# Kernel tuning notes

Measured on AMD Instinct MI355X. Metric: run time of the kernel, lower is better.

## Reference

```python
import jax, jax.numpy as jnp
import numpy as np

# Phi-3-small blocksparse config
S = 2048            # num prompt tokens (single sequence)
H = 32              # num query heads
HKV = 8             # num kv heads (GQA)
D = 128             # head size
BLK = 64            # sparse_block_size
LOCAL = 16          # local_blocks
VERT = 8            # vert_stride
SCALE = 0.08838834764831845  # 1/sqrt(128)
HEAD_SLIDE = max(1, VERT // H)  # = 1 (per-head vertical offset, homo_head=False)


def _blocksparse_mask():
    """Per-head local+strided block-sparse causal mask, shape [H, S, S] bool."""
    nb = S // BLK
    qb = jnp.arange(nb)[None, :, None]   # query block idx
    kb = jnp.arange(nb)[None, None, :]   # key block idx
    h = jnp.arange(H)[:, None, None]
    blk = (qb >= kb) & (
        (qb - kb < LOCAL) | (((kb + h * HEAD_SLIDE + 1) % VERT) == 0)
    )  # [H, nb, nb]
    dense = jnp.repeat(jnp.repeat(blk, BLK, axis=1), BLK, axis=2)  # [H, S, S]
    causal = jnp.arange(S)[:, None] >= jnp.arange(S)[None, :]
    return dense & causal[None]


def setup_inputs() -> dict:
    key = jax.random.key(0)
    k1, k2, k3 = jax.random.split(key, 3)
    return {
        "query": jax.random.normal(k1, (S, H * D), dtype=jnp.float32),
        "key": jax.random.normal(k2, (S, HKV * D), dtype=jnp.float32),
        "value": jax.random.normal(k3, (S, HKV * D), dtype=jnp.float32),
    }


def reference(query, key, value):
    q = query.reshape(S, H, D)
    k = jnp.repeat(key.reshape(S, HKV, D), H // HKV, axis=1)    # GQA expand
    v = jnp.repeat(value.reshape(S, HKV, D), H // HKV, axis=1)
    scores = jnp.einsum("qhd,khd->hqk", q, k) * SCALE           # [H, S, S]
    mask = _blocksparse_mask()
    scores = jnp.where(mask, scores, jnp.finfo(scores.dtype).min)
    p = jax.nn.softmax(scores, axis=-1)
    out = jnp.einsum("hqk,khd->qhd", p, v)                      # [S, H, D]
    return out.reshape(S, H * D)
```

## Files before the change

kernel.cpp:

```cpp
#include <hip/hip_runtime.h>


typedef __bf16 bf16_t;
typedef __bf16 bf16x4 __attribute__((ext_vector_type(4)));
typedef __bf16 bf16x8 __attribute__((ext_vector_type(8)));
typedef float  fx4    __attribute__((ext_vector_type(4)));

#define SL2E_F 0.1275240614354876f

__device__ inline void load_lds16(const bf16_t* g, bf16_t* l) {
    __builtin_amdgcn_global_load_lds(
        (const __attribute__((address_space(1))) void*)g,
        (__attribute__((address_space(3))) void*)l, 16, 0, 0);
}

__global__ void prep_kernel(const float* __restrict__ K, const float* __restrict__ V,
                            bf16_t* __restrict__ Kb, bf16_t* __restrict__ VT)
{
    const int blk = blockIdx.x;
    {
        const size_t base = (size_t)blk * 4096 + (size_t)threadIdx.x * 16;
        fx4 a0 = *(const fx4*)(K + base);
        fx4 a1 = *(const fx4*)(K + base + 4);
        fx4 a2 = *(const fx4*)(K + base + 8);
        fx4 a3 = *(const fx4*)(K + base + 12);
        bf16x8 f0, f1;
        f0[0]=(bf16_t)a0[0]; f0[1]=(bf16_t)a0[1]; f0[2]=(bf16_t)a0[2]; f0[3]=(bf16_t)a0[3];
        f0[4]=(bf16_t)a1[0]; f0[5]=(bf16_t)a1[1]; f0[6]=(bf16_t)a1[2]; f0[7]=(bf16_t)a1[3];
        f1[0]=(bf16_t)a2[0]; f1[1]=(bf16_t)a2[1]; f1[2]=(bf16_t)a2[2]; f1[3]=(bf16_t)a2[3];
        f1[4]=(bf16_t)a3[0]; f1[5]=(bf16_t)a3[1]; f1[6]=(bf16_t)a3[2]; f1[7]=(bf16_t)a3[3];
        *(bf16x8*)(Kb + base)     = f0;
        *(bf16x8*)(Kb + base + 8) = f1;
    }
    __shared__ __align__(16) bf16_t T[64 * 72];
    const int s0 = (blk & 31) * 64;
    const int c0 = (blk >> 5) * 64;
    const int tx = threadIdx.x & 15, ty = threadIdx.x >> 4;
    fx4 a0 = *(const fx4*)(V + (size_t)(s0 + ty * 4 + 0) * 1024 + c0 + tx * 4);
    fx4 a1 = *(const fx4*)(V + (size_t)(s0 + ty * 4 + 1) * 1024 + c0 + tx * 4);
    fx4 a2 = *(const fx4*)(V + (size_t)(s0 + ty * 4 + 2) * 1024 + c0 + tx * 4);
    fx4 a3 = *(const fx4*)(V + (size_t)(s0 + ty * 4 + 3) * 1024 + c0 + tx * 4);
#pragma unroll
    for (int j = 0; j < 4; ++j) {
        bf16x4 f = { (bf16_t)a0[j], (bf16_t)a1[j], (bf16_t)a2[j], (bf16_t)a3[j] };
        *(bf16x4*)&T[(tx * 4 + j) * 72 + ty * 4] = f;
    }
    __syncthreads();
    const int c = threadIdx.x >> 2, part = threadIdx.x & 3;
    bf16x8 x0 = *(const bf16x8*)&T[c * 72 + part * 16];
    bf16x8 x1 = *(const bf16x8*)&T[c * 72 + part * 16 + 8];
    bf16_t* dst = VT + (size_t)(c0 + c) * 2048 + s0 + part * 16;
    *(bf16x8*)(dst)     = x0;
    *(bf16x8*)(dst + 8) = x1;
}

__launch_bounds__(128, 2)
__global__ void bsfa_kernel(const float* __restrict__ Q,
                            const bf16_t* __restrict__ Kb,
                            const bf16_t* __restrict__ VT,
                            float* __restrict__ O)
{
    const int blk  = blockIdx.x;
    const int kvh  = blk & 7;
    const int h    = kvh * 4 + ((blk >> 3) & 3);
    const int qb   = 31 - (blk >> 5);
    const int tid  = threadIdx.x;
    const int rh   = tid >> 6;
    const int lane = tid & 63;
    const int l15  = lane & 15;
    const int quad = lane >> 4;

    __shared__ __align__(16) bf16_t Ks[64 * 128];
    __shared__ __align__(16) bf16_t Vs[128 * 64];

    bf16_t* Pt = &Ks[rh * 2304];

    const int row0 = qb * 64 + rh * 32;

    const bf16_t* kg = Kb + (size_t)kvh * 128;
    const bf16_t* vg = VT + ((size_t)kvh * 128) * 2048;

    bf16x8 qf[2][4];
#pragma unroll
    for (int qt = 0; qt < 2; ++qt) {
        const float* qp = Q + (size_t)(row0 + qt * 16 + l15) * 4096 + h * 128;
#pragma unroll
        for (int kc = 0; kc < 4; ++kc) {
            fx4 a = *(const fx4*)(qp + kc * 32 + quad * 8);
            fx4 b = *(const fx4*)(qp + kc * 32 + quad * 8 + 4);
            bf16x8 f;
            f[0] = (bf16_t)(a[0] * SL2E_F); f[1] = (bf16_t)(a[1] * SL2E_F);
            f[2] = (bf16_t)(a[2] * SL2E_F); f[3] = (bf16_t)(a[3] * SL2E_F);
            f[4] = (bf16_t)(b[0] * SL2E_F); f[5] = (bf16_t)(b[1] * SL2E_F);
            f[6] = (bf16_t)(b[2] * SL2E_F); f[7] = (bf16_t)(b[3] * SL2E_F);
            qf[qt][kc] = f;
        }
    }

    bf16x8 ones;
#pragma unroll
    for (int i = 0; i < 8; ++i) ones[i] = (bf16_t)1.0f;

    fx4 oacc[8][2];
    fx4 lacc[2];
    const fx4 zero4 = {0.0f, 0.0f, 0.0f, 0.0f};
#pragma unroll
    for (int dt = 0; dt < 8; ++dt)
#pragma unroll
        for (int qt = 0; qt < 2; ++qt)
            oacc[dt][qt] = zero4;
    lacc[0] = zero4; lacc[1] = zero4;

    for (int kb = 0; kb <= qb; ++kb) {
        if (!((qb - kb < 16) || (((kb + h + 1) & 7) == 0))) continue;

        {
            const bf16_t* kt_g = kg + ((size_t)kb << 16);
            const bf16_t* vt_g = vg + ((size_t)kb << 6);
#pragma unroll
            for (int i = 0; i < 8; ++i) {
                const int chunk = i * 128 + tid;
                const int krow = chunk >> 4;
                const int kc   = (chunk & 15) ^ (krow & 15);
                load_lds16(kt_g + (size_t)krow * 1024 + kc * 8, Ks + (size_t)chunk * 8);
                const int vrow = chunk >> 3;
                const int vc   = (chunk & 7) ^ (vrow & 7);
                load_lds16(vt_g + (size_t)vrow * 2048 + vc * 8, Vs + (size_t)chunk * 8);
            }
        }
        __syncthreads();

        fx4 sacc[4][2];
#pragma unroll
        for (int kt = 0; kt < 4; ++kt)
#pragma unroll
            for (int qt = 0; qt < 2; ++qt)
                sacc[kt][qt] = zero4;
#pragma unroll
        for (int kc = 0; kc < 4; ++kc)
#pragma unroll
            for (int kt = 0; kt < 4; ++kt) {
                bf16x8 kf = *(const bf16x8*)&Ks[(kt * 16 + l15) * 128 + (((kc * 4 + quad) ^ l15)) * 8];
#pragma unroll
                for (int qt = 0; qt < 2; ++qt)
                    sacc[kt][qt] = __builtin_amdgcn_mfma_f32_16x16x32_bf16(
                        kf, qf[qt][kc], sacc[kt][qt], 0, 0, 0);
            }

        if (kb == qb) {
#pragma unroll
            for (int kt = 0; kt < 4; ++kt)
#pragma unroll
                for (int qt = 0; qt < 2; ++qt)
#pragma unroll
                    for (int r = 0; r < 4; ++r) {
                        const int k_in = kt * 16 + quad * 4 + r;
                        const int q_in = rh * 32 + qt * 16 + l15;
                        if (q_in < k_in) sacc[kt][qt][r] = -1e30f;
                    }
        }

#pragma unroll
        for (int kt = 0; kt < 4; ++kt)
#pragma unroll
            for (int qt = 0; qt < 2; ++qt)
#pragma unroll
                for (int r = 0; r < 4; ++r)
                    sacc[kt][qt][r] = exp2f(sacc[kt][qt][r]);

        __syncthreads();

#pragma unroll
        for (int qt = 0; qt < 2; ++qt)
#pragma unroll
            for (int kt = 0; kt < 4; ++kt) {
                bf16x4 f = { (bf16_t)sacc[kt][qt][0], (bf16_t)sacc[kt][qt][1],
                             (bf16_t)sacc[kt][qt][2], (bf16_t)sacc[kt][qt][3] };
                *(bf16x4*)&Pt[(qt * 16 + l15) * 72 + kt * 16 + quad * 4] = f;
            }
        __asm__ __volatile__("s_waitcnt lgkmcnt(0)" ::: "memory");

        bf16x8 pf[2][2];
#pragma unroll
        for (int qt = 0; qt < 2; ++qt)
#pragma unroll
            for (int kcg = 0; kcg < 2; ++kcg)
                pf[qt][kcg] = *(const bf16x8*)&Pt[(qt * 16 + l15) * 72 + kcg * 32 + quad * 8];

#pragma unroll
        for (int kcg = 0; kcg < 2; ++kcg) {
#pragma unroll
            for (int dt = 0; dt < 8; ++dt) {
                bf16x8 vf = *(const bf16x8*)&Vs[(dt * 16 + l15) * 64 + (((kcg * 4 + quad) ^ (l15 & 7))) * 8];
#pragma unroll
                for (int qt = 0; qt < 2; ++qt)
                    oacc[dt][qt] = __builtin_amdgcn_mfma_f32_16x16x32_bf16(
                        vf, pf[qt][kcg], oacc[dt][qt], 0, 0, 0);
            }
#pragma unroll
            for (int qt = 0; qt < 2; ++qt)
                lacc[qt] = __builtin_amdgcn_mfma_f32_16x16x32_bf16(
                    ones, pf[qt][kcg], lacc[qt], 0, 0, 0);
        }

        __syncthreads();
    }

    const float inv0 = 1.0f / lacc[0][0];
    const float inv1 = 1.0f / lacc[1][0];
#pragma unroll
    for (int dt = 0; dt < 8; ++dt)
#pragma unroll
        for (int qt = 0; qt < 2; ++qt) {
            const float inv = qt ? inv1 : inv0;
            fx4 o = oacc[dt][qt] * inv;
            *(fx4*)(O + (size_t)(row0 + qt * 16 + l15) * 4096 + h * 128 + dt * 16 + quad * 4) = o;
        }
}

extern "C" void kernel_launch(void* const* d_in, const int* in_sizes, int n_in,
                              void* d_out, int out_size, void* d_ws, size_t ws_size,
                              hipStream_t stream) {
    (void)in_sizes; (void)n_in; (void)ws_size; (void)out_size;
    const float* q = (const float*)d_in[0];
    const float* k = (const float*)d_in[1];
    const float* v = (const float*)d_in[2];
    float* o = (float*)d_out;

    bf16_t* Kb = (bf16_t*)d_ws;
    bf16_t* VT = Kb + (size_t)2048 * 1024;

    prep_kernel<<<dim3(512), dim3(256), 0, stream>>>(k, v, Kb, VT);
    bsfa_kernel<<<dim3(1024), dim3(128), 0, stream>>>(q, Kb, VT, o);
}
```

Measured before the change: 138.7 us.

## Enumerate active key blocks directly and prefetch next K/V tile during PV MMA

Replaces the scan over all key blocks with a direct iterator that visits only active blocks: strided vertical blocks first, then the local window. All V fragments are read into registers before a barrier, so the next tile's global-to-LDS loads can be issued while the PV MFMAs run on register data. This overlaps memory traffic with compute. In exchange it adds 16 bf16x8 registers per thread, which may pressure occupancy at the 2-waves launch bound.

```diff
diff --git a/kernel.cpp b/kernel.cpp
--- a/kernel.cpp
+++ b/kernel.cpp
@@ -111,24 +111,34 @@
             oacc[dt][qt] = zero4;
     lacc[0] = zero4; lacc[1] = zero4;
 
-    for (int kb = 0; kb <= qb; ++kb) {
-        if (!((qb - kb < 16) || (((kb + h + 1) & 7) == 0))) continue;
-
-        {
-            const bf16_t* kt_g = kg + ((size_t)kb << 16);
-            const bf16_t* vt_g = vg + ((size_t)kb << 6);
-#pragma unroll
-            for (int i = 0; i < 8; ++i) {
-                const int chunk = i * 128 + tid;
-                const int krow = chunk >> 4;
-                const int kc   = (chunk & 15) ^ (krow & 15);
-                load_lds16(kt_g + (size_t)krow * 1024 + kc * 8, Ks + (size_t)chunk * 8);
-                const int vrow = chunk >> 3;
-                const int vc   = (chunk & 7) ^ (vrow & 7);
-                load_lds16(vt_g + (size_t)vrow * 2048 + vc * 8, Vs + (size_t)chunk * 8);
-            }
-        }
-        __syncthreads();
+    auto stage = [&](int t) {
+        const bf16_t* kt_g = kg + ((size_t)t << 16);
+        const bf16_t* vt_g = vg + ((size_t)t << 6);
+#pragma unroll
+        for (int i = 0; i < 8; ++i) {
+            const int chunk = i * 128 + tid;
+            const int krow = chunk >> 4;
+            const int kc   = (chunk & 15) ^ (krow & 15);
+            load_lds16(kt_g + (size_t)krow * 1024 + kc * 8, Ks + (size_t)chunk * 8);
+            const int vrow = chunk >> 3;
+            const int vc   = (chunk & 7) ^ (vrow & 7);
+            load_lds16(vt_g + (size_t)vrow * 2048 + vc * 8, Vs + (size_t)chunk * 8);
+        }
+    };
+
+    const int loc0 = (qb > 15) ? (qb - 15) : 0;
+    const int kb0s = (8 - ((h + 1) & 7)) & 7;
+    auto nxt = [&](int kb) -> int {
+        if (kb < loc0) { const int t = kb + 8; return (t <= qb - 16) ? t : loc0; }
+        return (kb < qb) ? (kb + 1) : -1;
+    };
+
+    int kb = (qb - 16 >= kb0s) ? kb0s : loc0;
+    stage(kb);
+    __syncthreads();
+
+    while (kb >= 0) {
+        const int nkb = nxt(kb);
 
         fx4 sacc[4][2];
 #pragma unroll
@@ -179,6 +189,7 @@
                 *(bf16x4*)&Pt[(qt * 16 + l15) * 72 + kt * 16 + quad * 4] = f;
             }
         __asm__ __volatile__("s_waitcnt lgkmcnt(0)" ::: "memory");
+        __builtin_amdgcn_sched_barrier(0);
 
         bf16x8 pf[2][2];
 #pragma unroll
@@ -186,17 +197,25 @@
 #pragma unroll
             for (int kcg = 0; kcg < 2; ++kcg)
                 pf[qt][kcg] = *(const bf16x8*)&Pt[(qt * 16 + l15) * 72 + kcg * 32 + quad * 8];
+        bf16x8 vf[2][8];
+#pragma unroll
+        for (int kcg = 0; kcg < 2; ++kcg)
+#pragma unroll
+            for (int dt = 0; dt < 8; ++dt)
+                vf[kcg][dt] = *(const bf16x8*)&Vs[(dt * 16 + l15) * 64 + (((kcg * 4 + quad) ^ (l15 & 7))) * 8];
+
+        __syncthreads();
+
+        if (nkb >= 0) stage(nkb);
 
 #pragma unroll
         for (int kcg = 0; kcg < 2; ++kcg) {
 #pragma unroll
-            for (int dt = 0; dt < 8; ++dt) {
-                bf16x8 vf = *(const bf16x8*)&Vs[(dt * 16 + l15) * 64 + (((kcg * 4 + quad) ^ (l15 & 7))) * 8];
+            for (int dt = 0; dt < 8; ++dt)
 #pragma unroll
                 for (int qt = 0; qt < 2; ++qt)
                     oacc[dt][qt] = __builtin_amdgcn_mfma_f32_16x16x32_bf16(
-                        vf, pf[qt][kcg], oacc[dt][qt], 0, 0, 0);
-            }
+                        vf[kcg][dt], pf[qt][kcg], oacc[dt][qt], 0, 0, 0);
 #pragma unroll
             for (int qt = 0; qt < 2; ++qt)
                 lacc[qt] = __builtin_amdgcn_mfma_f32_16x16x32_bf16(
@@ -204,6 +223,7 @@
         }
 
         __syncthreads();
+        kb = nkb;
     }
 
     const float inv0 = 1.0f / lacc[0][0];
```

After: 159.8 us. 1.15x slower.
